# Kernel optimization log

Hardware: AMD Instinct MI355X
Metric: run time of the kernel (lower is better)

## Reference

```python
import jax, jax.numpy as jnp
import numpy as np

XI = 4.0  # init kwarg


def _gaussian_kernel(xi: float):
    radius = int(3 * xi)
    coords = jnp.arange(-radius, radius + 1, dtype=jnp.float32)
    g1 = jnp.exp(-coords ** 2 / (2 * xi * xi))
    g1 = g1 / g1.sum()
    # dense 3D outer-product kernel, shape (K, K, K)
    g3 = g1[:, None, None] * g1[None, :, None] * g1[None, None, :]
    K = g3.shape[0]
    # grouped depthwise weight: (out=3, in/groups=1, K, K, K)
    return jnp.broadcast_to(g3[None, None], (3, 1, K, K, K))


def setup_inputs() -> dict:
    key = jax.random.key(0)
    x = jax.random.normal(key, (1, 3, 160, 160, 160), dtype=jnp.float32)
    kernel = _gaussian_kernel(XI)
    return {"x": x, "kernel": kernel}


def reference(x, kernel):
    # grouped Conv3d, groups=3 (depthwise), 'same' padding of radius each side
    r = (kernel.shape[-1] - 1) // 2
    return jax.lax.conv_general_dilated(
        x, kernel,
        window_strides=(1, 1, 1),
        padding=[(r, r), (r, r), (r, r)],
        dimension_numbers=("NCDHW", "OIDHW", "NCDHW"),
        feature_group_count=3,
    )
```

## Files before the change

kernel.cpp:

```cpp
#include <hip/hip_runtime.h>
#include <hip/hip_fp16.h>


#define NV 160
constexpr int KS    = 25;
constexpr int RAD   = 12;
constexpr int PLANE = NV * NV;
constexpr int VOL   = NV * NV * NV;
constexpr int TOT   = 3 * VOL;

constexpr int WHR   = 16;
constexpr int WPIT  = 189;
constexpr int OPT   = 10;
constexpr int WIN   = OPT + KS - 1;

constexpr int HC2   = 80;
constexpr int TR    = HC2 + 2 * RAD;
constexpr int TP2   = 84;
constexpr int NTASK = TR * 20;

__device__ __forceinline__ void pk(float2& a, float2 g, float2 v) {
    asm("v_pk_fma_f32 %0, %1, %2, %0" : "+v"(a) : "v"(g), "v"(v));
}

__device__ __forceinline__ void load_g(const float* __restrict__ k3, float* g) {
    float c   = k3[12 * 625 + 312];
    float g12 = cbrtf(c);
    float inv = 1.0f / (g12 * g12);
#pragma unroll
    for (int t = 0; t < KS; ++t) g[t] = k3[t * 625 + 312] * inv;
}

__global__ __launch_bounds__(256) void conv_w(const float* __restrict__ in,
                                              __half* __restrict__ out,
                                              const float* __restrict__ k3) {
    __shared__ float X[WHR][WPIT];
    float g[KS];
    load_g(k3, g);

    int tid = threadIdx.x;
    int b   = blockIdx.x;
    int hc  = b % 10;
    int cd  = b / 10;
    int h0  = hc * WHR;
    const float* base = in + (size_t)cd * PLANE + (size_t)h0 * NV;

    for (int z = tid; z < WHR * 24; z += 256) {
        int r = z / 24, u = z % 24;
        X[r][u < 12 ? u : 160 + u] = 0.f;
    }
#pragma unroll
    for (int it = 0; it < 3; ++it) {
        int task = it * 256 + tid;
        if (task < WHR * 40) {
            int q = task % 40, r = task / 40;
            float4 f = *(const float4*)(base + r * NV + 4 * q);
            X[r][12 + 4 * q]     = f.x;
            X[r][12 + 4 * q + 1] = f.y;
            X[r][12 + 4 * q + 2] = f.z;
            X[r][12 + 4 * q + 3] = f.w;
        }
    }
    __syncthreads();

    int c = tid & 15;
    int r = tid >> 4;
    float acc[OPT];
#pragma unroll
    for (int j = 0; j < OPT; ++j) acc[j] = 0.f;
#pragma unroll
    for (int it = 0; it < WIN; ++it) {
        float v = X[r][c * OPT + it];
#pragma unroll
        for (int j = 0; j < OPT; ++j) {
            int t = it - j;
            if (t >= 0 && t < KS) acc[j] = fmaf(g[t], v, acc[j]);
        }
    }
    __half* ob = out + (size_t)cd * PLANE + (size_t)(h0 + r) * NV + c * OPT;
#pragma unroll
    for (int j = 0; j < OPT / 2; ++j)
        *(__half2*)(ob + 2 * j) =
            __float22half2_rn(make_float2(acc[2 * j], acc[2 * j + 1]));
}

__global__ __launch_bounds__(320) void conv_h(const __half* __restrict__ in,
                                              __half* __restrict__ out,
                                              const float* __restrict__ k3) {
    __shared__ __half2 T[TR][TP2];
    float gs[KS];
    load_g(k3, gs);
    float2 g2[KS];
#pragma unroll
    for (int t = 0; t < KS; ++t) g2[t] = make_float2(gs[t], gs[t]);

    int tid = threadIdx.x;
    int b   = blockIdx.x;
    int hh  = b & 1;
    int cd  = b >> 1;
    int h0  = hh * HC2;
    const __half* base = in + (size_t)cd * PLANE;

#pragma unroll
    for (int it = 0; it < 7; ++it) {
        int task = it * 320 + tid;
        if (task < NTASK) {
            int r = task / 20, k = task % 20;
            int hg = h0 - RAD + r;
            uint4 v = make_uint4(0u, 0u, 0u, 0u);
            if (hg >= 0 && hg < NV)
                v = *(const uint4*)(base + hg * NV + 8 * k);
            *(uint4*)(&T[r][4 * k]) = v;
        }
    }
    __syncthreads();

    int wp = tid % 80, oc = tid / 80;
#pragma unroll
    for (int hv = 0; hv < 2; ++hv) {
        int rb = (oc + 4 * hv) * OPT;
        float2 acc[OPT];
#pragma unroll
        for (int j = 0; j < OPT; ++j) acc[j] = make_float2(0.f, 0.f);
#pragma unroll
        for (int it = 0; it < WIN; ++it) {
            float2 v = __half22float2(T[rb + it][wp]);
#pragma unroll
            for (int j = 0; j < OPT; ++j) {
                int t = it - j;
                if (t >= 0 && t < KS) pk(acc[j], g2[t], v);
            }
        }
        __half* op = out + (size_t)cd * PLANE + (size_t)(h0 + rb) * NV + 2 * wp;
#pragma unroll
        for (int j = 0; j < OPT; ++j)
            *(__half2*)(op + j * NV) = __float22half2_rn(acc[j]);
    }
}

__global__ __launch_bounds__(320) void conv_d(const __half* __restrict__ in,
                                              float* __restrict__ out,
                                              const float* __restrict__ k3) {
    __shared__ __half2 T[TR][TP2];
    float gs[KS];
    load_g(k3, gs);
    float2 g2[KS];
#pragma unroll
    for (int t = 0; t < KS; ++t) g2[t] = make_float2(gs[t], gs[t]);

    int tid = threadIdx.x;
    int b   = blockIdx.x;
    int dh  = b & 1;
    int ch  = b >> 1;
    int c   = ch / NV, h = ch % NV;
    int d0  = dh * HC2;
    const __half* base = in + (size_t)c * VOL + h * NV;

#pragma unroll
    for (int it = 0; it < 7; ++it) {
        int task = it * 320 + tid;
        if (task < NTASK) {
            int r = task / 20, k = task % 20;
            int dg = d0 - RAD + r;
            uint4 v = make_uint4(0u, 0u, 0u, 0u);
            if (dg >= 0 && dg < NV)
                v = *(const uint4*)(base + (size_t)dg * PLANE + 8 * k);
            *(uint4*)(&T[r][4 * k]) = v;
        }
    }
    __syncthreads();

    int wp = tid % 80, oc = tid / 80;
#pragma unroll
    for (int hv = 0; hv < 2; ++hv) {
        int rb = (oc + 4 * hv) * OPT;
        float2 acc[OPT];
#pragma unroll
        for (int j = 0; j < OPT; ++j) acc[j] = make_float2(0.f, 0.f);
#pragma unroll
        for (int it = 0; it < WIN; ++it) {
            float2 v = __half22float2(T[rb + it][wp]);
#pragma unroll
            for (int j = 0; j < OPT; ++j) {
                int t = it - j;
                if (t >= 0 && t < KS) pk(acc[j], g2[t], v);
            }
        }
        float* op = out + (size_t)c * VOL + h * NV + 2 * wp;
#pragma unroll
        for (int j = 0; j < OPT; ++j)
            *(float2*)(op + (size_t)(d0 + rb + j) * PLANE) = acc[j];
    }
}

__global__ __launch_bounds__(256) void conv3d_direct(const float* __restrict__ x,
                                                     const float* __restrict__ k3,
                                                     float* __restrict__ out) {
    int idx = blockIdx.x * 256 + threadIdx.x;
    if (idx >= TOT) return;
    int w = idx % NV;
    int t = idx / NV;
    int h = t % NV; t /= NV;
    int d = t % NV;
    int c = t / NV;
    const float* kc = k3 + c * (KS * KS * KS);
    float acc = 0.f;
    for (int i = 0; i < KS; ++i) {
        int dd = d + i - RAD;
        if (dd < 0 || dd >= NV) continue;
        for (int j = 0; j < KS; ++j) {
            int hh = h + j - RAD;
            if (hh < 0 || hh >= NV) continue;
            const float* xr = x + (c * NV + dd) * NV * NV + hh * NV + (w - RAD);
            const float* kr = kc + (i * KS + j) * KS;
            int k0 = (RAD - w) > 0 ? (RAD - w) : 0;
            int k1 = (NV + RAD - w) < KS ? (NV + RAD - w) : KS;
            for (int k = k0; k < k1; ++k) acc += kr[k] * xr[k];
        }
    }
    out[idx] = acc;
}

extern "C" void kernel_launch(void* const* d_in, const int* in_sizes, int n_in,
                              void* d_out, int out_size, void* d_ws, size_t ws_size,
                              hipStream_t stream) {
    const float* x  = (const float*)d_in[0];
    const float* k3 = (const float*)d_in[1];
    float* out = (float*)d_out;

    if (ws_size >= (size_t)TOT * 2 * sizeof(__half)) {
        __half* tmpA = (__half*)d_ws;
        __half* tmpB = tmpA + TOT;
        conv_w<<<480 * 10, 256, 0, stream>>>(x, tmpA, k3);
        conv_h<<<480 * 2, 320, 0, stream>>>(tmpA, tmpB, k3);
        conv_d<<<480 * 2, 320, 0, stream>>>(tmpB, out, k3);
    } else {
        conv3d_direct<<<(TOT + 255) / 256, 256, 0, stream>>>(x, k3, out);
    }
}
```

Measured before the change: 56.35 us.

## Fuse W and H separable passes into one kernel with symmetric taps

Merges the width and height 1D Gaussian passes into a single kernel that loads a 104-row halo slab into shared memory as half precision, runs the W pass into a second shared buffer, then runs the H pass from it. This removes one fp16 intermediate volume round trip through global memory and one kernel launch. Tap weights are also held as 13 symmetric values instead of 25 to lower register use. In exchange, the W pass is recomputed on the 24 halo rows of each block, the input is rounded to half before the first pass, and shared memory per block grows.

```diff
diff --git a/kernel.cpp b/kernel.cpp
--- a/kernel.cpp
+++ b/kernel.cpp
@@ -9,132 +9,120 @@
 constexpr int VOL   = NV * NV * NV;
 constexpr int TOT   = 3 * VOL;
 
-constexpr int WHR   = 16;
-constexpr int WPIT  = 189;
+constexpr int FH  = 80;
+constexpr int FR  = 104;
+constexpr int XP  = 198;
+constexpr int WPT = 170;
+
+constexpr int HC2   = 80;
+constexpr int TR    = 104;
+constexpr int TP2   = 84;
+constexpr int NTASK = TR * 20;
 constexpr int OPT   = 10;
 constexpr int WIN   = OPT + KS - 1;
 
-constexpr int HC2   = 80;
-constexpr int TR    = HC2 + 2 * RAD;
-constexpr int TP2   = 84;
-constexpr int NTASK = TR * 20;
+#define GW(t)  g[(t) < 13 ? (t) : 24 - (t)]
+#define GW2(t) g2[(t) < 13 ? (t) : 24 - (t)]
 
 __device__ __forceinline__ void pk(float2& a, float2 g, float2 v) {
     asm("v_pk_fma_f32 %0, %1, %2, %0" : "+v"(a) : "v"(g), "v"(v));
 }
 
-__device__ __forceinline__ void load_g(const float* __restrict__ k3, float* g) {
+__device__ __forceinline__ void load_g13(const float* __restrict__ k3, float* g) {
     float c   = k3[12 * 625 + 312];
     float g12 = cbrtf(c);
     float inv = 1.0f / (g12 * g12);
 #pragma unroll
-    for (int t = 0; t < KS; ++t) g[t] = k3[t * 625 + 312] * inv;
-}
-
-__global__ __launch_bounds__(256) void conv_w(const float* __restrict__ in,
-                                              __half* __restrict__ out,
-                                              const float* __restrict__ k3) {
-    __shared__ float X[WHR][WPIT];
-    float g[KS];
-    load_g(k3, g);
-
-    int tid = threadIdx.x;
-    int b   = blockIdx.x;
-    int hc  = b % 10;
-    int cd  = b / 10;
-    int h0  = hc * WHR;
-    const float* base = in + (size_t)cd * PLANE + (size_t)h0 * NV;
-
-    for (int z = tid; z < WHR * 24; z += 256) {
-        int r = z / 24, u = z % 24;
-        X[r][u < 12 ? u : 160 + u] = 0.f;
-    }
-#pragma unroll
-    for (int it = 0; it < 3; ++it) {
-        int task = it * 256 + tid;
-        if (task < WHR * 40) {
-            int q = task % 40, r = task / 40;
-            float4 f = *(const float4*)(base + r * NV + 4 * q);
-            X[r][12 + 4 * q]     = f.x;
-            X[r][12 + 4 * q + 1] = f.y;
-            X[r][12 + 4 * q + 2] = f.z;
-            X[r][12 + 4 * q + 3] = f.w;
-        }
-    }
-    __syncthreads();
-
-    int c = tid & 15;
-    int r = tid >> 4;
-    float acc[OPT];
-#pragma unroll
-    for (int j = 0; j < OPT; ++j) acc[j] = 0.f;
-#pragma unroll
-    for (int it = 0; it < WIN; ++it) {
-        float v = X[r][c * OPT + it];
-#pragma unroll
-        for (int j = 0; j < OPT; ++j) {
-            int t = it - j;
-            if (t >= 0 && t < KS) acc[j] = fmaf(g[t], v, acc[j]);
-        }
-    }
-    __half* ob = out + (size_t)cd * PLANE + (size_t)(h0 + r) * NV + c * OPT;
-#pragma unroll
-    for (int j = 0; j < OPT / 2; ++j)
-        *(__half2*)(ob + 2 * j) =
-            __float22half2_rn(make_float2(acc[2 * j], acc[2 * j + 1]));
-}
-
-__global__ __launch_bounds__(320) void conv_h(const __half* __restrict__ in,
-                                              __half* __restrict__ out,
-                                              const float* __restrict__ k3) {
-    __shared__ __half2 T[TR][TP2];
-    float gs[KS];
-    load_g(k3, gs);
-    float2 g2[KS];
-#pragma unroll
-    for (int t = 0; t < KS; ++t) g2[t] = make_float2(gs[t], gs[t]);
+    for (int t = 0; t < 13; ++t) g[t] = k3[t * 625 + 312] * inv;
+}
+
+__global__ __launch_bounds__(512, 4) void fused_wh(const float* __restrict__ in,
+                                                   __half* __restrict__ out,
+                                                   const float* __restrict__ k3) {
+    __shared__ __half X[FR][XP];
+    __shared__ __half WB[FR][WPT];
+    float g[13];
+    load_g13(k3, g);
 
     int tid = threadIdx.x;
     int b   = blockIdx.x;
     int hh  = b & 1;
     int cd  = b >> 1;
-    int h0  = hh * HC2;
-    const __half* base = in + (size_t)cd * PLANE;
-
-#pragma unroll
-    for (int it = 0; it < 7; ++it) {
-        int task = it * 320 + tid;
-        if (task < NTASK) {
-            int r = task / 20, k = task % 20;
+    int h0  = hh * FH;
+    const float* base = in + (size_t)cd * PLANE;
+
+    const __half2 Z2 = __float22half2_rn(make_float2(0.f, 0.f));
+    for (int z = tid; z < FR * 12; z += 512) {
+        int r = z / 12, u = z % 12;
+        int col = (u < 6) ? 2 * u : 172 + 2 * (u - 6);
+        *(__half2*)&X[r][col] = Z2;
+    }
+#pragma unroll
+    for (int it = 0; it < 9; ++it) {
+        int task = it * 512 + tid;
+        if (task < FR * 40) {
+            int r = task / 40, q = task % 40;
             int hg = h0 - RAD + r;
-            uint4 v = make_uint4(0u, 0u, 0u, 0u);
+            float4 f = make_float4(0.f, 0.f, 0.f, 0.f);
             if (hg >= 0 && hg < NV)
-                v = *(const uint4*)(base + hg * NV + 8 * k);
-            *(uint4*)(&T[r][4 * k]) = v;
+                f = *(const float4*)(base + hg * NV + 4 * q);
+            *(__half2*)&X[r][12 + 4 * q]     = __float22half2_rn(make_float2(f.x, f.y));
+            *(__half2*)&X[r][12 + 4 * q + 2] = __float22half2_rn(make_float2(f.z, f.w));
         }
     }
     __syncthreads();
 
-    int wp = tid % 80, oc = tid / 80;
-#pragma unroll
-    for (int hv = 0; hv < 2; ++hv) {
-        int rb = (oc + 4 * hv) * OPT;
-        float2 acc[OPT];
-#pragma unroll
-        for (int j = 0; j < OPT; ++j) acc[j] = make_float2(0.f, 0.f);
-#pragma unroll
-        for (int it = 0; it < WIN; ++it) {
-            float2 v = __half22float2(T[rb + it][wp]);
-#pragma unroll
-            for (int j = 0; j < OPT; ++j) {
-                int t = it - j;
-                if (t >= 0 && t < KS) pk(acc[j], g2[t], v);
+#pragma unroll
+    for (int it2 = 0; it2 < 2; ++it2) {
+        int task = it2 * 512 + tid;
+        if (task < FR * 8) {
+            int cc = task & 7, r = task >> 3;
+            float acc[20];
+#pragma unroll
+            for (int j = 0; j < 20; ++j) acc[j] = 0.f;
+#pragma unroll
+            for (int s = 0; s < 44; ++s) {
+                float v = __half2float(X[r][20 * cc + s]);
+#pragma unroll
+                for (int j = 0; j < 20; ++j) {
+                    int t = s - j;
+                    if (t >= 0 && t < KS) acc[j] = fmaf(GW(t), v, acc[j]);
+                }
             }
-        }
-        __half* op = out + (size_t)cd * PLANE + (size_t)(h0 + rb) * NV + 2 * wp;
-#pragma unroll
-        for (int j = 0; j < OPT; ++j)
-            *(__half2*)(op + j * NV) = __float22half2_rn(acc[j]);
+#pragma unroll
+            for (int j = 0; j < 10; ++j)
+                *(__half2*)&WB[r][20 * cc + 2 * j] =
+                    __float22half2_rn(make_float2(acc[2 * j], acc[2 * j + 1]));
+        }
+    }
+    __syncthreads();
+
+    float2 g2[13];
+#pragma unroll
+    for (int t = 0; t < 13; ++t) g2[t] = make_float2(g[t], g[t]);
+#pragma unroll
+    for (int it2 = 0; it2 < 2; ++it2) {
+        int task = it2 * 512 + tid;
+        if (task < 640) {
+            int wp = task % 80, hc = task / 80;
+            int hb = hc * 10;
+            float2 acc[10];
+#pragma unroll
+            for (int j = 0; j < 10; ++j) acc[j] = make_float2(0.f, 0.f);
+#pragma unroll
+            for (int s = 0; s < 34; ++s) {
+                float2 v = __half22float2(*(__half2*)&WB[hb + s][2 * wp]);
+#pragma unroll
+                for (int j = 0; j < 10; ++j) {
+                    int t = s - j;
+                    if (t >= 0 && t < KS) pk(acc[j], GW2(t), v);
+                }
+            }
+            __half* op = out + (size_t)cd * PLANE + (size_t)(h0 + hb) * NV + 2 * wp;
+#pragma unroll
+            for (int j = 0; j < 10; ++j)
+                *(__half2*)(op + j * NV) = __float22half2_rn(acc[j]);
+        }
     }
 }
 
@@ -142,11 +130,11 @@
                                               float* __restrict__ out,
                                               const float* __restrict__ k3) {
     __shared__ __half2 T[TR][TP2];
-    float gs[KS];
-    load_g(k3, gs);
-    float2 g2[KS];
-#pragma unroll
-    for (int t = 0; t < KS; ++t) g2[t] = make_float2(gs[t], gs[t]);
+    float g[13];
+    load_g13(k3, g);
+    float2 g2[13];
+#pragma unroll
+    for (int t = 0; t < 13; ++t) g2[t] = make_float2(g[t], g[t]);
 
     int tid = threadIdx.x;
     int b   = blockIdx.x;
@@ -183,7 +171,7 @@
 #pragma unroll
             for (int j = 0; j < OPT; ++j) {
                 int t = it - j;
-                if (t >= 0 && t < KS) pk(acc[j], g2[t], v);
+                if (t >= 0 && t < KS) pk(acc[j], GW2(t), v);
             }
         }
         float* op = out + (size_t)c * VOL + h * NV + 2 * wp;
@@ -228,12 +216,10 @@
     const float* k3 = (const float*)d_in[1];
     float* out = (float*)d_out;
 
-    if (ws_size >= (size_t)TOT * 2 * sizeof(__half)) {
+    if (ws_size >= (size_t)TOT * sizeof(__half)) {
         __half* tmpA = (__half*)d_ws;
-        __half* tmpB = tmpA + TOT;
-        conv_w<<<480 * 10, 256, 0, stream>>>(x, tmpA, k3);
-        conv_h<<<480 * 2, 320, 0, stream>>>(tmpA, tmpB, k3);
-        conv_d<<<480 * 2, 320, 0, stream>>>(tmpB, out, k3);
+        fused_wh<<<960, 512, 0, stream>>>(x, tmpA, k3);
+        conv_d<<<960, 320, 0, stream>>>(tmpA, out, k3);
     } else {
         conv3d_direct<<<(TOT + 255) / 256, 256, 0, stream>>>(x, k3, out);
     }
```

After: 58.61 us. 1.04x slower.
